# Optimization experiments

Hardware: AMD Instinct MI355X
Metric: run time of the kernel (lower is better)

The kernel has to match this reference:

```python
import jax, jax.numpy as jnp
import numpy as np

B, HT, WD, DIM = 8, 128, 128, 512
NUM_HEADS = 8
HEAD_DIM = DIM // NUM_HEADS
K = 7  # kernel_size
R = K // 2


def setup_inputs() -> dict:
    key = jax.random.key(0)
    k1, k2 = jax.random.split(key)
    x = jax.random.normal(k1, (B, HT, WD, DIM), dtype=jnp.float32)
    # nn.Linear(dim, 2*dim, bias=False); stored as [in, out] so y = x @ W_qk
    W_qk = jax.random.normal(k2, (DIM, 2 * DIM), dtype=jnp.float32) * (DIM ** -0.5)
    return {"x": x, "W_qk": W_qk}


def reference(x, W_qk):
    Bsz, H, W, C = x.shape
    scale = HEAD_DIM ** -0.5
    # qk projection -> [B,H,W,2,heads,head_dim]
    qk = (x @ W_qk).reshape(Bsz, H, W, 2, NUM_HEADS, HEAD_DIM)
    q = qk[..., 0, :, :] * scale          # [B,H,W,hd,d]
    kk = qk[..., 1, :, :]                 # [B,H,W,hd,d]
    # NATTEN border handling: window start clamped so the KxK window stays inside.
    starts_i = jnp.clip(jnp.arange(H) - R, 0, H - K)  # [H]
    starts_j = jnp.clip(jnp.arange(W) - R, 0, W - K)  # [W]
    attn = []
    for ki in range(K):
        k_row = kk[:, starts_i + ki]          # [B,H,W,hd,d] (gather rows)
        for kj in range(K):
            k_n = k_row[:, :, starts_j + kj]  # [B,H,W,hd,d] (gather cols)
            attn.append(jnp.einsum('bhwnd,bhwnd->bhwn', q, k_n))
    attn = jnp.stack(attn, axis=-1)           # [B,H,W,hd,K*K]
    return jnp.transpose(attn, (0, 3, 1, 2, 4))  # [B,hd,H,W,K*K]
```

## Files before the change

kernel.cpp:

```cpp
#include <hip/hip_runtime.h>

typedef __attribute__((ext_vector_type(8))) short short8;
typedef __attribute__((ext_vector_type(4))) float floatx4;

__device__ __forceinline__ unsigned short f2bf(float f) {
  union { float f; unsigned u; } x; x.f = f;
  unsigned u = x.u + 0x7fffu + ((x.u >> 16) & 1u);
  return (unsigned short)(u >> 16);
}

__device__ __forceinline__ void gload_lds16(const void* g, void* l) {
  __builtin_amdgcn_global_load_lds(
      (const __attribute__((address_space(1))) unsigned int*)g,
      (__attribute__((address_space(3))) unsigned int*)l, 16, 0, 0);
}


__global__ __launch_bounds__(256) void cvt_x(const float4* __restrict__ x,
                                             uint2* __restrict__ o) {
  size_t idx = (size_t)blockIdx.x * 256 + threadIdx.x;
  float4 v = x[idx];
  uint2 r;
  r.x = (unsigned)f2bf(v.x) | ((unsigned)f2bf(v.y) << 16);
  r.y = (unsigned)f2bf(v.z) | ((unsigned)f2bf(v.w) << 16);
  o[idx] = r;
}

__global__ __launch_bounds__(256) void cvt_w(const float* __restrict__ w,
                                             unsigned short* __restrict__ wt) {
  int tid = blockIdx.x * 256 + threadIdx.x;
  int n = tid >> 9, k = tid & 511;
  float v = w[k * 1024 + n];
  if (n < 512) v *= 0.125f;
  wt[tid] = f2bf(v);
}

__global__ __launch_bounds__(256) void gemm_bt(const unsigned short* __restrict__ A,
                                               const unsigned short* __restrict__ Bt,
                                               unsigned short* __restrict__ C) {
  __shared__ __align__(16) unsigned short lds_a[4 * 128 * 8];
  __shared__ __align__(16) unsigned short lds_b[4 * 128 * 8];

  const int t = threadIdx.x;
  const int bid = blockIdx.x;
  const int wg = (bid & 7) * 1024 + (bid >> 3);
  const int mtile = wg >> 3;
  const int ntile = wg & 7;
  const int m0 = mtile * 128, n0 = ntile * 128;
  const int wave = t >> 6, lane = t & 63;
  const int wm = (wave & 1) * 64, wn = (wave >> 1) * 64;
  const int kg = lane >> 4, rr = lane & 15;

  floatx4 acc[4][4] = {};

  for (int k0 = 0; k0 < 512; k0 += 32) {
#pragma unroll
    for (int s = 0; s < 2; ++s) {
      int S = t + s * 256;
      int kgrp = S >> 7, row = S & 127;
      gload_lds16(&A[(size_t)(m0 + row) * 512 + k0 + kgrp * 8], &lds_a[S * 8]);
      gload_lds16(&Bt[(size_t)(n0 + row) * 512 + k0 + kgrp * 8], &lds_b[S * 8]);
    }
    __syncthreads();

    short8 af[4], bf[4];
#pragma unroll
    for (int i = 0; i < 4; ++i) {
      af[i] = *(const short8*)&lds_a[(kg * 128 + wm + i * 16 + rr) * 8];
      bf[i] = *(const short8*)&lds_b[(kg * 128 + wn + i * 16 + rr) * 8];
    }
#pragma unroll
    for (int i = 0; i < 4; ++i)
#pragma unroll
      for (int j = 0; j < 4; ++j)
        acc[i][j] = __builtin_amdgcn_mfma_f32_16x16x32_bf16(af[i], bf[j], acc[i][j], 0, 0, 0);
    __syncthreads();
  }

#pragma unroll
  for (int i = 0; i < 4; ++i) {
    int mrow = m0 + wm + i * 16 + (lane >> 4) * 4;
#pragma unroll
    for (int j = 0; j < 4; ++j) {
      int ncol = n0 + wn + j * 16 + (lane & 15);
#pragma unroll
      for (int r = 0; r < 4; ++r)
        C[(size_t)(mrow + r) * 1024 + ncol] = f2bf(acc[i][j][r]);
    }
  }
}

__global__ __launch_bounds__(256) void attn_mfma(const unsigned short* __restrict__ QK,
                                                 float* __restrict__ out) {
  __shared__ __align__(16) unsigned short q_lds[128 * 64];
  __shared__ __align__(16) unsigned short k_lds[2][128 * 64];
  __shared__ __align__(16) float s_scr[4][24 * 20];
  __shared__ __align__(16) float out_lds[128 * 49];

  const int t = threadIdx.x;
  const int bid = blockIdx.x;
  const int wg = (bid & 7) * 1024 + (bid >> 3);
  const int i = wg & 127;
  const int h = (wg >> 7) & 7;
  const int b = wg >> 10;
  const int wave = t >> 6, lane = t & 63;
  const int kg = lane >> 4, rr = lane & 15;
  const int ri = min(max(i - 3, 0), 121);

  const unsigned short* qbase = QK + ((size_t)(b * 128 + i) * 128) * 1024 + h * 64;
#pragma unroll
  for (int s = 0; s < 4; ++s) {
    int S = t + s * 256;
    int j = S >> 3, pg = S & 7, lg = pg ^ (j & 7);
    gload_lds16(qbase + (size_t)j * 1024 + lg * 8, &q_lds[S * 8]);
  }
  {
    const unsigned short* kb = QK + ((size_t)(b * 128 + ri) * 128) * 1024 + 512 + h * 64;
#pragma unroll
    for (int s = 0; s < 4; ++s) {
      int S = t + s * 256;
      int c = S >> 3, pg = S & 7, lg = pg ^ (c & 7);
      gload_lds16(kb + (size_t)c * 1024 + lg * 8, &k_lds[0][S * 8]);
    }
  }
  __syncthreads();

  short8 af[2][2];
#pragma unroll
  for (int jt2 = 0; jt2 < 2; ++jt2) {
    int row = (wave * 2 + jt2) * 16 + rr;
#pragma unroll
    for (int ks = 0; ks < 2; ++ks) {
      int lg = ks * 4 + kg;
      af[jt2][ks] = *(const short8*)&q_lds[(row * 8 + (lg ^ (row & 7))) * 8];
    }
  }

  const int m = lane >> 2, kj0 = lane & 3;

  for (int ki = 0; ki < 7; ++ki) {
    const int cur = ki & 1;
    if (ki < 6) {
      const unsigned short* kb =
          QK + ((size_t)(b * 128 + ri + ki + 1) * 128) * 1024 + 512 + h * 64;
#pragma unroll
      for (int s = 0; s < 4; ++s) {
        int S = t + s * 256;
        int c = S >> 3, pg = S & 7, lg = pg ^ (c & 7);
        gload_lds16(kb + (size_t)c * 1024 + lg * 8, &k_lds[cur ^ 1][S * 8]);
      }
    }
    const unsigned short* kbuf = k_lds[cur];
    float* scr = s_scr[wave];

#pragma unroll
    for (int jt2 = 0; jt2 < 2; ++jt2) {
      const int j0 = (wave * 2 + jt2) * 16;
      const int cb = min(max(j0 - 3, 0), 121);
      const int c0 = min(cb + rr, 127);
      const int c1 = min(cb + 16 + rr, 127);
      floatx4 acc0 = {0.f, 0.f, 0.f, 0.f}, acc1 = {0.f, 0.f, 0.f, 0.f};
#pragma unroll
      for (int ks = 0; ks < 2; ++ks) {
        int lg = ks * 4 + kg;
        short8 b0 = *(const short8*)&kbuf[(c0 * 8 + (lg ^ (c0 & 7))) * 8];
        short8 b1 = *(const short8*)&kbuf[(c1 * 8 + (lg ^ (c1 & 7))) * 8];
        acc0 = __builtin_amdgcn_mfma_f32_16x16x32_bf16(af[jt2][ks], b0, acc0, 0, 0, 0);
        acc1 = __builtin_amdgcn_mfma_f32_16x16x32_bf16(af[jt2][ks], b1, acc1, 0, 0, 0);
      }
      {
        int crow = (lane >> 4) * 4;
        *(floatx4*)&scr[rr * 20 + crow] = acc0;
        if (rr < 8) *(floatx4*)&scr[(16 + rr) * 20 + crow] = acc1;
      }
      asm volatile("s_waitcnt lgkmcnt(0)" ::: "memory");
      {
        int relc = min(max(j0 + m - 3, 0), 121) - cb;
        int p = j0 + m;
        out_lds[p * 49 + ki * 7 + kj0] = scr[(relc + kj0) * 20 + m];
        if (kj0 < 3)
          out_lds[p * 49 + ki * 7 + 4 + kj0] = scr[(relc + 4 + kj0) * 20 + m];
      }
      asm volatile("s_waitcnt lgkmcnt(0)" ::: "memory");
    }
    __syncthreads();
  }

  const uint4* src = (const uint4*)out_lds;
  uint4* dst = (uint4*)(out + ((size_t)(b * 8 + h) * 16384 + (size_t)i * 128) * 49);
  for (int s = t; s < 1568; s += 256) dst[s] = src[s];
}

extern "C" void kernel_launch(void* const* d_in, const int* in_sizes, int n_in,
                              void* d_out, int out_size, void* d_ws, size_t ws_size,
                              hipStream_t stream) {
  const float* x = (const float*)d_in[0];
  const float* w = (const float*)d_in[1];
  float* out = (float*)d_out;

  unsigned short* xb = (unsigned short*)d_ws;
  unsigned short* wt = xb + 67108864;
  unsigned short* qk = wt + 524288;

  cvt_x<<<65536, 256, 0, stream>>>((const float4*)x, (uint2*)xb);
  cvt_w<<<2048, 256, 0, stream>>>(w, wt);
  gemm_bt<<<8192, 256, 0, stream>>>(xb, wt, qk);
  attn_mfma<<<8192, 256, 0, stream>>>(qk, out);
}
```

Baseline: 851.9 us.

## Double-buffer LDS tiles in projection GEMM to overlap loads with MFMA

The GEMM's A and B LDS tiles become two ping-pong buffers. The next k-slice is prefetched with global_load_lds while MFMAs run on the current slice, so only one barrier per step is needed instead of two. Per-thread base pointers are hoisted out of the loop and the loop is kept rolled. This costs twice the LDS for the GEMM and relies on the single barrier to order the async LDS writes against reads.

```diff
diff --git a/kernel.cpp b/kernel.cpp
--- a/kernel.cpp
+++ b/kernel.cpp
@@ -38,8 +38,8 @@
 __global__ __launch_bounds__(256) void gemm_bt(const unsigned short* __restrict__ A,
                                                const unsigned short* __restrict__ Bt,
                                                unsigned short* __restrict__ C) {
-  __shared__ __align__(16) unsigned short lds_a[4 * 128 * 8];
-  __shared__ __align__(16) unsigned short lds_b[4 * 128 * 8];
+  __shared__ __align__(16) unsigned short lds_a[2][4 * 128 * 8];
+  __shared__ __align__(16) unsigned short lds_b[2][4 * 128 * 8];
 
   const int t = threadIdx.x;
   const int bid = blockIdx.x;
@@ -51,30 +51,46 @@
   const int wm = (wave & 1) * 64, wn = (wave >> 1) * 64;
   const int kg = lane >> 4, rr = lane & 15;
 
+  const int Skgrp0 = t >> 7, Srow0 = t & 127;
+  const int Skgrp1 = (t + 256) >> 7, Srow1 = t & 127;
+  const unsigned short* a0 = &A[(size_t)(m0 + Srow0) * 512 + Skgrp0 * 8];
+  const unsigned short* a1 = &A[(size_t)(m0 + Srow1) * 512 + Skgrp1 * 8];
+  const unsigned short* b0 = &Bt[(size_t)(n0 + Srow0) * 512 + Skgrp0 * 8];
+  const unsigned short* b1 = &Bt[(size_t)(n0 + Srow1) * 512 + Skgrp1 * 8];
+
   floatx4 acc[4][4] = {};
 
-  for (int k0 = 0; k0 < 512; k0 += 32) {
-#pragma unroll
-    for (int s = 0; s < 2; ++s) {
-      int S = t + s * 256;
-      int kgrp = S >> 7, row = S & 127;
-      gload_lds16(&A[(size_t)(m0 + row) * 512 + k0 + kgrp * 8], &lds_a[S * 8]);
-      gload_lds16(&Bt[(size_t)(n0 + row) * 512 + k0 + kgrp * 8], &lds_b[S * 8]);
-    }
-    __syncthreads();
+  gload_lds16(a0, &lds_a[0][t * 8]);
+  gload_lds16(b0, &lds_b[0][t * 8]);
+  gload_lds16(a1, &lds_a[0][(t + 256) * 8]);
+  gload_lds16(b1, &lds_b[0][(t + 256) * 8]);
+  __syncthreads();
+
+  int cur = 0;
+#pragma unroll 1
+  for (int step = 0; step < 16; ++step) {
+    if (step < 15) {
+      int k0n = (step + 1) * 32;
+      gload_lds16(a0 + k0n, &lds_a[cur ^ 1][t * 8]);
+      gload_lds16(b0 + k0n, &lds_b[cur ^ 1][t * 8]);
+      gload_lds16(a1 + k0n, &lds_a[cur ^ 1][(t + 256) * 8]);
+      gload_lds16(b1 + k0n, &lds_b[cur ^ 1][(t + 256) * 8]);
+    }
 
     short8 af[4], bf[4];
 #pragma unroll
     for (int i = 0; i < 4; ++i) {
-      af[i] = *(const short8*)&lds_a[(kg * 128 + wm + i * 16 + rr) * 8];
-      bf[i] = *(const short8*)&lds_b[(kg * 128 + wn + i * 16 + rr) * 8];
+      af[i] = *(const short8*)&lds_a[cur][(kg * 128 + wm + i * 16 + rr) * 8];
+      bf[i] = *(const short8*)&lds_b[cur][(kg * 128 + wn + i * 16 + rr) * 8];
     }
 #pragma unroll
     for (int i = 0; i < 4; ++i)
 #pragma unroll
       for (int j = 0; j < 4; ++j)
         acc[i][j] = __builtin_amdgcn_mfma_f32_16x16x32_bf16(af[i], bf[j], acc[i][j], 0, 0, 0);
+
     __syncthreads();
+    cur ^= 1;
   }
 
 #pragma unroll
```

Result: no change. 851.0 us (-0.1%).

## Enlarge GEMM tile to 256x256 with double-buffered K=64 LDS pipeline

Applied to the files above, without the earlier changes.

The QK projection GEMM moves from 128x128 tiles with 4 waves and a single-buffered K=32 loop to 256x256 tiles with 8 waves, each wave computing a 128x64 sub-tile. K steps are now 64 wide and use a double-buffered LDS prefetch, so the next tile's global loads overlap the MFMA work and only one barrier is needed per step. The larger tiles are meant to cut global and LDS traffic per FLOP and remove redundant reloads. In exchange, register pressure rises to 32 accumulators per wave and LDS use per block grows to 128KB, which can reduce occupancy.

```diff
diff --git a/kernel.cpp b/kernel.cpp
--- a/kernel.cpp
+++ b/kernel.cpp
@@ -35,54 +35,78 @@
   wt[tid] = f2bf(v);
 }
 
-__global__ __launch_bounds__(256) void gemm_bt(const unsigned short* __restrict__ A,
-                                               const unsigned short* __restrict__ Bt,
-                                               unsigned short* __restrict__ C) {
-  __shared__ __align__(16) unsigned short lds_a[4 * 128 * 8];
-  __shared__ __align__(16) unsigned short lds_b[4 * 128 * 8];
+__global__ __launch_bounds__(512, 2) void gemm_bt(const unsigned short* __restrict__ A,
+                                                  const unsigned short* __restrict__ Bt,
+                                                  unsigned short* __restrict__ C) {
+  __shared__ __align__(16) unsigned short lds_a[2][8 * 256 * 8];
+  __shared__ __align__(16) unsigned short lds_b[2][8 * 256 * 8];
 
   const int t = threadIdx.x;
   const int bid = blockIdx.x;
-  const int wg = (bid & 7) * 1024 + (bid >> 3);
-  const int mtile = wg >> 3;
-  const int ntile = wg & 7;
-  const int m0 = mtile * 128, n0 = ntile * 128;
+  const int wg = (bid & 7) * 256 + (bid >> 3);
+  const int mtile = wg >> 2;
+  const int ntile = wg & 3;
+  const int m0 = mtile * 256, n0 = ntile * 256;
   const int wave = t >> 6, lane = t & 63;
-  const int wm = (wave & 1) * 64, wn = (wave >> 1) * 64;
+  const int wm = (wave >> 2) * 128, wn = (wave & 3) * 64;
   const int kg = lane >> 4, rr = lane & 15;
 
-  floatx4 acc[4][4] = {};
-
-  for (int k0 = 0; k0 < 512; k0 += 32) {
-#pragma unroll
-    for (int s = 0; s < 2; ++s) {
-      int S = t + s * 256;
-      int kgrp = S >> 7, row = S & 127;
-      gload_lds16(&A[(size_t)(m0 + row) * 512 + k0 + kgrp * 8], &lds_a[S * 8]);
-      gload_lds16(&Bt[(size_t)(n0 + row) * 512 + k0 + kgrp * 8], &lds_b[S * 8]);
-    }
+  const unsigned short* aptr[4];
+  const unsigned short* bptr[4];
+#pragma unroll
+  for (int p = 0; p < 4; ++p) {
+    int S = t + p * 512, kgrp = S >> 8, row = S & 255;
+    aptr[p] = &A[(size_t)(m0 + row) * 512 + kgrp * 8];
+    bptr[p] = &Bt[(size_t)(n0 + row) * 512 + kgrp * 8];
+  }
+
+#pragma unroll
+  for (int p = 0; p < 4; ++p) {
+    gload_lds16(aptr[p], &lds_a[0][(t + p * 512) * 8]);
+    gload_lds16(bptr[p], &lds_b[0][(t + p * 512) * 8]);
+  }
+  __syncthreads();
+
+  floatx4 acc[8][4] = {};
+  int cur = 0;
+#pragma unroll 1
+  for (int step = 0; step < 8; ++step) {
+    if (step < 7) {
+      int k0n = (step + 1) * 64;
+#pragma unroll
+      for (int p = 0; p < 4; ++p) {
+        gload_lds16(aptr[p] + k0n, &lds_a[cur ^ 1][(t + p * 512) * 8]);
+        gload_lds16(bptr[p] + k0n, &lds_b[cur ^ 1][(t + p * 512) * 8]);
+      }
+    }
+
+#pragma unroll
+    for (int kc = 0; kc < 2; ++kc) {
+      const int kbase = (kc * 4 + kg) * 256;
+      short8 af[8], bf[4];
+#pragma unroll
+      for (int i = 0; i < 8; ++i)
+        af[i] = *(const short8*)&lds_a[cur][(kbase + wm + i * 16 + rr) * 8];
+#pragma unroll
+      for (int j = 0; j < 4; ++j)
+        bf[j] = *(const short8*)&lds_b[cur][(kbase + wn + j * 16 + rr) * 8];
+#pragma unroll
+      for (int i = 0; i < 8; ++i)
+#pragma unroll
+        for (int j = 0; j < 4; ++j)
+          acc[i][j] = __builtin_amdgcn_mfma_f32_16x16x32_bf16(af[i], bf[j], acc[i][j], 0, 0, 0);
+    }
+
     __syncthreads();
-
-    short8 af[4], bf[4];
-#pragma unroll
-    for (int i = 0; i < 4; ++i) {
-      af[i] = *(const short8*)&lds_a[(kg * 128 + wm + i * 16 + rr) * 8];
-      bf[i] = *(const short8*)&lds_b[(kg * 128 + wn + i * 16 + rr) * 8];
-    }
-#pragma unroll
-    for (int i = 0; i < 4; ++i)
-#pragma unroll
-      for (int j = 0; j < 4; ++j)
-        acc[i][j] = __builtin_amdgcn_mfma_f32_16x16x32_bf16(af[i], bf[j], acc[i][j], 0, 0, 0);
-    __syncthreads();
-  }
-
-#pragma unroll
-  for (int i = 0; i < 4; ++i) {
+    cur ^= 1;
+  }
+
+#pragma unroll
+  for (int i = 0; i < 8; ++i) {
     int mrow = m0 + wm + i * 16 + (lane >> 4) * 4;
 #pragma unroll
     for (int j = 0; j < 4; ++j) {
-      int ncol = n0 + wn + j * 16 + (lane & 15);
+      int ncol = n0 + wn + j * 16 + rr;
 #pragma unroll
       for (int r = 0; r < 4; ++r)
         C[(size_t)(mrow + r) * 1024 + ncol] = f2bf(acc[i][j][r]);
@@ -204,6 +228,6 @@
 
   cvt_x<<<65536, 256, 0, stream>>>((const float4*)x, (uint2*)xb);
   cvt_w<<<2048, 256, 0, stream>>>(w, wt);
-  gemm_bt<<<8192, 256, 0, stream>>>(xb, wt, qk);
+  gemm_bt<<<2048, 512, 0, stream>>>(xb, wt, qk);
   attn_mfma<<<8192, 256, 0, stream>>>(qk, out);
 }
```

New measurement: 875.3 us. 1.03x slower.
